# Kernel optimization log

Measured on AMD Instinct MI355X. Metric: run time of the kernel, lower is better.

## Reference

```python
import jax, jax.numpy as jnp
import numpy as np

NUM_HEADS = 32
EPS = 1e-5
NEG_INF = -1e9


def _ln(x, g, b):
    m = x.mean(-1, keepdims=True)
    v = ((x - m) ** 2).mean(-1, keepdims=True)
    return (x - m) / jnp.sqrt(v + EPS) * g + b


def setup_inputs() -> dict:
    key = jax.random.key(0)
    ks = jax.random.split(key, 20)
    N, B, D, E, F, L = 512, 2, 768, 256, 3072, 4
    inp = {
        'x': jax.random.normal(ks[0], (N, B, D), jnp.float32),
        'pos': jax.random.normal(ks[1], (B, N, 3), jnp.float32) * 5.0,
        'padding_mask': jnp.broadcast_to(jnp.arange(N)[None, :] >= N - 32, (B, N)),
        'outcell_index': jax.random.randint(ks[2], (B, E), 0, N),
        'expand_pos': jax.random.normal(ks[3], (B, E, 3), jnp.float32) * 5.0,
        'expand_mask': jnp.broadcast_to(jnp.arange(E)[None, :] >= E - 16, (B, E)),
        'vec_project_w': jax.random.normal(ks[4], (D, 3 * D), jnp.float32) * 0.02,
        'ln_x_g': jnp.ones((L, D), jnp.float32),
        'ln_x_b': jnp.zeros((L, D), jnp.float32),
        'ln_vec_g': jnp.ones((L, D), jnp.float32),
        'ln_vec_b': jnp.zeros((L, D), jnp.float32),
        'adaln_x_w': jax.random.normal(ks[5], (L, D, D), jnp.float32) * 0.02,
        'adaln_vecmlp_w': jax.random.normal(ks[6], (L, D, 2 * D), jnp.float32) * 0.02,
        'out_proj_w': jax.random.normal(ks[7], (L, D, D), jnp.float32) * 0.02,
        'vecmlp_norm_g': jnp.ones((L, D), jnp.float32),
        'vecmlp_norm_b': jnp.zeros((L, D), jnp.float32),
        'mlp_w1': jax.random.normal(ks[8], (L, D, F), jnp.float32) * 0.02,
        'mlp_w2': jax.random.normal(ks[9], (L, F, D), jnp.float32) * 0.02,
    }
    return inp


def reference(x, pos, padding_mask, outcell_index, expand_pos, expand_mask,
              vec_project_w, ln_x_g, ln_x_b, ln_vec_g, ln_vec_b,
              adaln_x_w, adaln_vecmlp_w, out_proj_w,
              vecmlp_norm_g, vecmlp_norm_b, mlp_w1, mlp_w2):
    x = jnp.swapaxes(x, 0, 1)  # [B,N,D]
    B, N, D = x.shape
    H = NUM_HEADS
    hd = D // H
    L = ln_x_g.shape[0]

    # --- PBC-expanded pairwise distance bias ---
    epf = jnp.concatenate([pos, expand_pos], axis=1)  # [B,S,3]
    S = epf.shape[1]
    delta = pos[:, :, None, :] - epf[:, None, :, :]   # [B,N,S,3]
    sq = (delta * delta).sum(-1)
    dist = jnp.where(sq > 0, jnp.sqrt(jnp.where(sq > 0, sq, 1.0)), 0.0)
    kpm_full = jnp.concatenate([padding_mask, expand_mask], axis=-1)  # [B,S]
    dist = jnp.where(padding_mask[:, :, None], 1e6, dist)
    dist = jnp.where(kpm_full[:, None, :], 1e6, dist)
    dist = 1.0 / (dist + 1.0)
    # additive attn mask (bias + key-padding -inf), broadcast over heads
    attn_mask = jnp.where(kpm_full[:, None, None, :], NEG_INF, dist[:, None, :, :])  # [B,1,N,S]

    vec = (jax.nn.silu(x) @ vec_project_w).reshape(B, N, 3, D)
    barange = jnp.arange(B)[:, None]
    scale = 1.0 / jnp.sqrt(jnp.float32(3 * hd))

    for l in range(L):
        rx, rv = x, vec
        xl = _ln(x, ln_x_g[l], ln_x_b[l])
        vl = _ln(vec, ln_vec_g[l], ln_vec_b[l])
        scale_x = jax.nn.silu(xl) @ adaln_x_w[l]        # [B,N,D]
        vmod = vl * scale_x[:, :, None, :]              # [B,N,3,D]
        # PBC gather-expanded K/V
        kv_exp = vmod[barange, outcell_index]           # [B,E,3,D]
        kv = jnp.concatenate([vmod, kv_exp], axis=1)    # [B,S,3,D]
        q = vmod.reshape(B, N, 3, H, hd).transpose(0, 3, 1, 2, 4).reshape(B, H, N, 3 * hd)
        k = kv.reshape(B, S, 3, H, hd).transpose(0, 3, 1, 2, 4).reshape(B, H, S, 3 * hd)
        v = k  # q=k=v in this block (same modulated vec)
        k = kv.reshape(B, S, 3, H, hd).transpose(0, 3, 1, 2, 4).reshape(B, H, S, 3 * hd)
        logits = jnp.einsum('bhnd,bhsd->bhns', q, k) * scale + attn_mask
        p = jax.nn.softmax(logits, axis=-1)
        o = jnp.einsum('bhns,bhsd->bhnd', p, v)          # [B,H,N,3hd]
        o = o.transpose(0, 2, 1, 3).reshape(B, N, H, 3, hd).transpose(0, 1, 3, 2, 4).reshape(B, N, 3, D)
        o = o @ out_proj_w[l]
        x = xl + rx
        vec = o + rv
        rx, rv = x, vec
        vm = _ln(vec, vecmlp_norm_g[l], vecmlp_norm_b[l])
        vm = jax.nn.silu(vm @ mlp_w1[l]) @ mlp_w2[l]     # [B,N,3,D]
        ss = jax.nn.silu(vm) @ adaln_vecmlp_w[l]         # [B,N,3,2D]
        sc, sh = jnp.split(ss, 2, axis=-1)
        x = x * sc.sum(-2) + sh.sum(-2) + rx
        vec = vm + rv
    return x, vec
```

## Files before the change

kernel.cpp:

```cpp
#include <hip/hip_runtime.h>

typedef __bf16 bf16_t;
typedef __bf16 bf8   __attribute__((ext_vector_type(8)));
typedef __bf16 bf4   __attribute__((ext_vector_type(4)));
typedef float  f32x4 __attribute__((ext_vector_type(4)));

__device__ __forceinline__ f32x4 mfma16(bf8 a, bf8 b, f32x4 c){
  return __builtin_amdgcn_mfma_f32_16x16x32_bf16(a, b, c, 0, 0, 0);
}
__device__ __forceinline__ float siluf_(float x){ return x / (1.f + __expf(-x)); }

__device__ __forceinline__ void async16(bf16_t* lds, const bf16_t* g){
  __builtin_amdgcn_global_load_lds(
      (const __attribute__((address_space(1))) unsigned int*)g,
      (__attribute__((address_space(3))) unsigned int*)lds, 16, 0, 0);
}

#define SCALE_QK 0.1178511302f

#define WT_VP   0ull
#define WT_AX   3538944ull
#define WT_AV   8257536ull
#define WT_OP   17694720ull
#define WT_M1   22413312ull
#define WT_M2   41287680ull
#define MASKB   60162048ull
#define SILUX   63307776ull
#define SILUXL  64880640ull
#define VLB     66453504ull
#define SCALEX  75890688ull
#define QKHB    79036416ull
#define KVTB    88473600ull
#define OBFB    97910784ull
#define VMLNB   102629376ull
#define H1B     107347968ull
#define SVM2B   126222336ull
#define SSB     130940928ull

struct TD { const float* s; bf16_t* d; int R, C, start, perz; };
struct TPack { TD t[6]; };

__global__ void transpose_all(TPack P)
{
  __shared__ bf16_t tile[64][66];
  const int bid = blockIdx.x;
  int k = 0;
  #pragma unroll
  for (int i = 1; i < 6; ++i) k = (bid >= P.t[i].start) ? i : k;
  const TD td = P.t[k];
  const int loc = bid - td.start;
  const int z = loc / td.perz, tl = loc - z*td.perz;
  const int nct = td.C >> 6;
  const int cx = tl % nct, ry = tl / nct;
  const size_t base = (size_t)z * td.R * td.C;
  const int r0 = ry*64, c0 = cx*64;
  const int tx = threadIdx.x, ty = threadIdx.y;
  #pragma unroll
  for (int j = 0; j < 16; ++j){
    int rr = ty + 4*j;
    tile[rr][tx] = (bf16_t)td.s[base + (size_t)(r0 + rr)*td.C + c0 + tx];
  }
  __syncthreads();
  #pragma unroll
  for (int j = 0; j < 16; ++j){
    int cc = ty + 4*j;
    td.d[base + (size_t)(c0 + cc)*td.R + r0 + tx] = tile[tx][cc];
  }
}

__global__ void mask_kernel(const float* __restrict__ pos, const float* __restrict__ epos,
                            bf16_t* __restrict__ wm)
{
  int i = blockIdx.x * 256 + threadIdx.x;
  int s = i % 768, t = i / 768;
  int n = t % 512, b = t / 512;
  bool kpm = (s < 512) ? (s >= 480) : (s >= 752);
  float o;
  if (kpm) o = 0.f;
  else {
    float d;
    if (n >= 480) d = 1e6f;
    else {
      const float* p = pos + (size_t)(b*512 + n)*3;
      const float* e = (s < 512) ? pos + (size_t)(b*512 + s)*3
                                 : epos + (size_t)(b*256 + (s-512))*3;
      float dx = p[0]-e[0], dy = p[1]-e[1], dz = p[2]-e[2];
      float sq = dx*dx + dy*dy + dz*dz;
      d = sq > 0.f ? sqrtf(sq) : 0.f;
    }
    o = __expf(1.f / (d + 1.f));
  }
  wm[i] = (bf16_t)o;
}

__global__ void xin_kernel(const float* __restrict__ xin, float* __restrict__ x,
                           bf16_t* __restrict__ sx)
{
  int i = blockIdx.x * 256 + threadIdx.x;
  int d = i % 768, t = i / 768;
  int n = t % 512, b = t / 512;
  float v = xin[((size_t)n*2 + b)*768 + d];
  x[i] = v;
  sx[i] = (bf16_t)siluf_(v);
}

__global__ __launch_bounds__(256,2) void ln_kernel(
    const float* __restrict__ in, const float* __restrict__ g, const float* __restrict__ bb,
    float* __restrict__ f32out, int addres, bf16_t* __restrict__ bfout, int dosilu)
{
  const int w = threadIdx.x >> 6, l = threadIdx.x & 63;
  const size_t r = (size_t)blockIdx.x * 4 + w;
  const float* p = in + r * 768;
  float v[12]; float s = 0.f;
  #pragma unroll
  for (int e = 0; e < 12; ++e){ v[e] = p[e*64 + l]; s += v[e]; }
  #pragma unroll
  for (int m = 1; m < 64; m <<= 1) s += __shfl_xor(s, m);
  float mean = s * (1.f/768.f);
  float q = 0.f;
  #pragma unroll
  for (int e = 0; e < 12; ++e){ float d = v[e] - mean; q += d*d; }
  #pragma unroll
  for (int m = 1; m < 64; m <<= 1) q += __shfl_xor(q, m);
  float rstd = rsqrtf(q * (1.f/768.f) + 1e-5f);
  #pragma unroll
  for (int e = 0; e < 12; ++e){
    int col = e*64 + l;
    float o = (v[e] - mean) * rstd * g[col] + bb[col];
    if (f32out) f32out[r*768 + col] = addres ? (o + v[e]) : o;
    if (bfout)  bfout[r*768 + col]  = (bf16_t)(dosilu ? siluf_(o) : o);
  }
}

__global__ __launch_bounds__(256,2) void pack2_kernel(
    const bf16_t* __restrict__ vl, const bf16_t* __restrict__ scx,
    const int* __restrict__ idx, bf16_t* __restrict__ qkh, bf16_t* __restrict__ kvt)
{
  __shared__ bf16_t tile[32*100];
  const int sb = blockIdx.x, bh = blockIdx.y;
  const int b = bh >> 5, h = bh & 31;
  const int tid = threadIdx.x;
  #pragma unroll
  for (int i = 0; i < 12; ++i){
    int e = i*256 + tid;
    int s_l = e / 96, col = e % 96;
    int s = sb*32 + s_l;
    float v = 0.f;
    if (col < 72){
      int n = (s < 512) ? s : idx[b*256 + (s - 512)];
      int c = col / 24, jj = col - c*24;
      int d = h*24 + jj;
      v = (float)vl[((size_t)(b*512 + n)*3 + c)*768 + d]
        * (float)scx[(size_t)(b*512 + n)*768 + d];
    }
    bf16_t bv = (bf16_t)v;
    qkh[((size_t)bh*768 + s)*96 + col] = bv;
    tile[s_l*100 + col] = bv;
  }
  __syncthreads();
  #pragma unroll
  for (int i = 0; i < 12; ++i){
    int f = i*256 + tid;
    int col = f >> 5, s_l = f & 31;
    kvt[((size_t)bh*96 + col)*768 + sb*32 + s_l] = tile[s_l*100 + col];
  }
}

__global__ __launch_bounds__(256,2) void attn_kernel(
    const bf16_t* __restrict__ qkh, const bf16_t* __restrict__ kvt,
    const bf16_t* __restrict__ wm, bf16_t* __restrict__ obf)
{
  __shared__ bf16_t Ks[64*128];
  __shared__ bf16_t Vs[96*72];
  __shared__ bf16_t Ps[64*72];
  const int g = blockIdx.x;
  const int qt = g >> 6, bh = g & 63;
  const int b = bh >> 5, h = bh & 31;
  const int tid = threadIdx.x, w = tid >> 6, l = tid & 63;
  const int lg = l >> 4, lr = l & 15;
  const int qn0 = qt*64 + w*16 + lg*4;

  bf8 aq[3];
  {
    const bf16_t* qb = qkh + ((size_t)bh*768 + qt*64 + w*16 + lr)*96;
    #pragma unroll
    for (int ks = 0; ks < 3; ++ks) aq[ks] = *(const bf8*)(qb + ks*32 + lg*8);
  }

  int klds[3], vlds[3]; size_t kg[3], vg[3];
  #pragma unroll
  for (int it = 0; it < 3; ++it){
    int f = it*256 + tid;
    int r_ = f / 12, c_ = f % 12;
    klds[it] = r_*256 + ((c_*16) ^ ((r_ & 7) << 4));
    kg[it] = ((size_t)bh*768 + r_)*96 + c_*8;
    int vd = f >> 3, vc = (f & 7)*8;
    vlds[it] = vd*72 + vc;
    vg[it] = ((size_t)bh*96 + vd)*768 + vc;
  }

  f32x4 zf = {0.f,0.f,0.f,0.f};
  f32x4 accO[6];
  #pragma unroll
  for (int i = 0; i < 6; ++i) accO[i] = zf;
  float m_r[4], s_r[4];
  #pragma unroll
  for (int r = 0; r < 4; ++r){ m_r[r] = -1e30f; s_r[r] = 0.f; }

  bf8 kr[3], vr[3];
  #pragma unroll
  for (int it = 0; it < 3; ++it){
    kr[it] = *(const bf8*)(qkh + kg[it]);
    vr[it] = *(const bf8*)(kvt + vg[it]);
  }
  #pragma unroll
  for (int it = 0; it < 3; ++it){
    *(bf8*)((char*)Ks + klds[it]) = kr[it];
    *(bf8*)&Vs[vlds[it]] = vr[it];
  }
  __syncthreads();

  const bf16_t* wrow = wm + (size_t)b*512*768;

  for (int t = 0; t < 12; ++t){
    const int s0 = t*64;
    if (t < 11){
      #pragma unroll
      for (int it = 0; it < 3; ++it){
        kr[it] = *(const bf8*)(qkh + kg[it] + (size_t)(s0 + 64)*96);
        vr[it] = *(const bf8*)(kvt + vg[it] + (s0 + 64));
      }
    }
    f32x4 sacc[4];
    __builtin_amdgcn_s_setprio(1);
    #pragma unroll
    for (int sf = 0; sf < 4; ++sf){
      sacc[sf] = zf;
      const int row = sf*16 + lr;
      #pragma unroll
      for (int ks = 0; ks < 3; ++ks){
        bf8 bg = *(const bf8*)((const char*)Ks + row*256 + ((ks*64 + lg*16) ^ ((row & 7) << 4)));
        sacc[sf] = mfma16(aq[ks], bg, sacc[sf]);
      }
    }
    __builtin_amdgcn_s_setprio(0);
    float tm[4];
    #pragma unroll
    for (int r = 0; r < 4; ++r)
      tm[r] = fmaxf(fmaxf(sacc[0][r], sacc[1][r]), fmaxf(sacc[2][r], sacc[3][r]));
    #pragma unroll
    for (int m = 1; m < 16; m <<= 1)
      #pragma unroll
      for (int r = 0; r < 4; ++r) tm[r] = fmaxf(tm[r], __shfl_xor(tm[r], m));
    float al[4], ps[4];
    #pragma unroll
    for (int r = 0; r < 4; ++r){
      float mn = fmaxf(m_r[r], tm[r]);
      al[r] = __expf((m_r[r] - mn)*SCALE_QK);
      m_r[r] = mn; ps[r] = 0.f;
    }
    #pragma unroll
    for (int sf = 0; sf < 4; ++sf)
      #pragma unroll
      for (int r = 0; r < 4; ++r){
        float p = __expf((sacc[sf][r] - m_r[r])*SCALE_QK)
                  * (float)wrow[(size_t)(qn0 + r)*768 + s0 + sf*16 + lr];
        ps[r] += p;
        Ps[(w*16 + lg*4 + r)*72 + sf*16 + lr] = (bf16_t)p;
      }
    #pragma unroll
    for (int m = 1; m < 16; m <<= 1)
      #pragma unroll
      for (int r = 0; r < 4; ++r) ps[r] += __shfl_xor(ps[r], m);
    #pragma unroll
    for (int r = 0; r < 4; ++r) s_r[r] = s_r[r]*al[r] + ps[r];
    #pragma unroll
    for (int df = 0; df < 6; ++df){
      f32x4 tt = accO[df];
      #pragma unroll
      for (int r = 0; r < 4; ++r) tt[r] *= al[r];
      accO[df] = tt;
    }
    __builtin_amdgcn_s_setprio(1);
    #pragma unroll
    for (int k2 = 0; k2 < 2; ++k2){
      bf8 pa = *(const bf8*)&Ps[(w*16 + lr)*72 + k2*32 + lg*8];
      #pragma unroll
      for (int df = 0; df < 6; ++df)
        accO[df] = mfma16(pa, *(const bf8*)&Vs[(df*16 + lr)*72 + k2*32 + lg*8], accO[df]);
    }
    __builtin_amdgcn_s_setprio(0);
    if (t < 11){
      __syncthreads();
      #pragma unroll
      for (int it = 0; it < 3; ++it){
        *(bf8*)((char*)Ks + klds[it]) = kr[it];
        *(bf8*)&Vs[vlds[it]] = vr[it];
      }
      __syncthreads();
    }
  }
  #pragma unroll
  for (int df = 0; df < 6; ++df){
    int dp = df*16 + lr;
    if (dp < 72){
      int c = dp / 24, jj = dp - c*24;
      #pragma unroll
      for (int r = 0; r < 4; ++r){
        float v = accO[df][r] / s_r[r];
        int qn = qn0 + r;
        obf[((size_t)(b*512 + qn)*3 + c)*768 + h*24 + jj] = (bf16_t)v;
      }
    }
  }
}

template<int EPI>
__global__ __launch_bounds__(512,4) void gemm2(
    const bf16_t* __restrict__ A, const bf16_t* __restrict__ Bt,
    float* __restrict__ Cf, bf16_t* __restrict__ Cb,
    int M, int Nn, int K, int Ksub, int ntiles)
{
  __shared__ bf16_t As[128*64];
  __shared__ bf16_t Bs[128*64];
  const int tid = threadIdx.x;
  const int w = tid >> 6, l = tid & 63;
  const int lg = l >> 4, lr = l & 15;
  const int gb = blockIdx.x;
  const int sidx = gb >> 3, xcd = gb & 7;
  const int nt = sidx % ntiles;
  const int mt = xcd + (sidx / ntiles) * 8;
  const int wm = (w >> 2) * 64, wn = (w & 3) * 32;

  const int srow = w*8 + (l >> 3);
  const int scol = (((l & 7) ^ (l >> 3)) << 3);
  const bf16_t* Ab = A  + (size_t)(mt*128) * K;
  const bf16_t* Bb = Bt + (size_t)(nt*128) * K;
  const int kbeg = blockIdx.z * Ksub;

  f32x4 zf = {0.f,0.f,0.f,0.f};
  f32x4 acc[4][2];
  #pragma unroll
  for (int i = 0; i < 4; ++i)
    #pragma unroll
    for (int j = 0; j < 2; ++j) acc[i][j] = zf;

  int offA[4], offB[2];
  #pragma unroll
  for (int i = 0; i < 4; ++i){
    int row = wm + i*16 + lr;
    offA[i] = row*128 + ((lg*16) ^ ((row & 7) << 4));
  }
  #pragma unroll
  for (int j = 0; j < 2; ++j){
    int row = wn + j*16 + lr;
    offB[j] = row*128 + ((lg*16) ^ ((row & 7) << 4));
  }

  for (int k0 = kbeg; k0 < kbeg + Ksub; k0 += 64){
    __syncthreads();
    #pragma unroll
    for (int c = 0; c < 2; ++c){
      async16(&As[c*4096 + w*512], Ab + (size_t)(c*64 + srow)*K + k0 + scol);
      async16(&Bs[c*4096 + w*512], Bb + (size_t)(c*64 + srow)*K + k0 + scol);
    }
    __syncthreads();
    #pragma unroll
    for (int kk = 0; kk < 2; ++kk){
      bf8 af[4], bg[2];
      #pragma unroll
      for (int i = 0; i < 4; ++i)
        af[i] = *(const bf8*)((const char*)As + (offA[i] ^ (kk*64)));
      #pragma unroll
      for (int j = 0; j < 2; ++j)
        bg[j] = *(const bf8*)((const char*)Bs + (offB[j] ^ (kk*64)));
      #pragma unroll
      for (int i = 0; i < 4; ++i)
        #pragma unroll
        for (int j = 0; j < 2; ++j)
          acc[i][j] = mfma16(af[i], bg[j], acc[i][j]);
    }
  }

  const size_t zoff = (EPI == 4) ? (size_t)blockIdx.z * M * Nn : 0;
  #pragma unroll
  for (int i = 0; i < 4; ++i){
    int r0 = mt*128 + wm + i*16 + lg*4;
    #pragma unroll
    for (int j = 0; j < 2; ++j){
      int cc = nt*128 + wn + j*16 + lr;
      #pragma unroll
      for (int r = 0; r < 4; ++r){
        size_t off = (size_t)(r0 + r)*Nn + cc;
        float v = acc[i][j][r];
        if constexpr (EPI == 0)      Cf[off] = v;
        else if constexpr (EPI == 2) Cb[off] = (bf16_t)siluf_(v);
        else if constexpr (EPI == 4) Cf[zoff + off] = v;
        else                         Cb[off] = (bf16_t)v;
      }
    }
  }
}

__global__ void reduce4_bf(const float* __restrict__ p, bf16_t* __restrict__ out)
{
  int i = blockIdx.x * 256 + threadIdx.x;
  const f32x4* p4 = (const f32x4*)p;
  f32x4 a = p4[i], b = p4[i + 196608], c = p4[i + 393216], d = p4[i + 589824];
  bf4 o;
  #pragma unroll
  for (int r = 0; r < 4; ++r) o[r] = (bf16_t)(a[r] + b[r] + c[r] + d[r]);
  ((bf4*)out)[i] = o;
}

__global__ __launch_bounds__(256,2) void redop_ln(
    const float* __restrict__ p, float* __restrict__ vec,
    const float* __restrict__ g, const float* __restrict__ bb,
    bf16_t* __restrict__ vmln)
{
  const int w = threadIdx.x >> 6, l = threadIdx.x & 63;
  const size_t r = (size_t)blockIdx.x * 4 + w;
  float v[12]; float s = 0.f;
  #pragma unroll
  for (int e = 0; e < 12; ++e){
    size_t off = r*768 + e*64 + l;
    float t = vec[off] + p[off] + p[off + 2359296];
    vec[off] = t;
    v[e] = t; s += t;
  }
  #pragma unroll
  for (int m = 1; m < 64; m <<= 1) s += __shfl_xor(s, m);
  float mean = s * (1.f/768.f);
  float q = 0.f;
  #pragma unroll
  for (int e = 0; e < 12; ++e){ float d = v[e] - mean; q += d*d; }
  #pragma unroll
  for (int m = 1; m < 64; m <<= 1) q += __shfl_xor(q, m);
  float rstd = rsqrtf(q * (1.f/768.f) + 1e-5f);
  #pragma unroll
  for (int e = 0; e < 12; ++e){
    int col = e*64 + l;
    vmln[r*768 + col] = (bf16_t)((v[e] - mean) * rstd * g[col] + bb[col]);
  }
}

__global__ void reduce_mlp2(const float* __restrict__ p, float* __restrict__ vec,
                            bf16_t* __restrict__ svm2)
{
  int i = blockIdx.x * 256 + threadIdx.x;
  const f32x4* p4 = (const f32x4*)p;
  f32x4 a = p4[i], b = p4[i + 589824];
  f32x4* v4 = (f32x4*)vec;
  f32x4 vv = v4[i];
  bf4 o;
  #pragma unroll
  for (int r = 0; r < 4; ++r){
    float s = a[r] + b[r];
    vv[r] += s;
    o[r] = (bf16_t)siluf_(s);
  }
  v4[i] = vv;
  ((bf4*)svm2)[i] = o;
}

__global__ __launch_bounds__(256,2) void comb_ln(
    const bf16_t* __restrict__ ss, float* __restrict__ x,
    const float* __restrict__ g, const float* __restrict__ bb,
    bf16_t* __restrict__ siluxl)
{
  const int w = threadIdx.x >> 6, l = threadIdx.x & 63;
  const size_t r = (size_t)blockIdx.x * 4 + w;
  const size_t base = r * 4608;
  float v[12]; float s = 0.f;
  #pragma unroll
  for (int e = 0; e < 12; ++e){
    int col = e*64 + l;
    float sc = (float)ss[base + col] + (float)ss[base + 1536 + col] + (float)ss[base + 3072 + col];
    float sh = (float)ss[base + 768 + col] + (float)ss[base + 2304 + col] + (float)ss[base + 3840 + col];
    float xv = x[r*768 + col]*(1.f + sc) + sh;
    v[e] = xv; s += xv;
  }
  #pragma unroll
  for (int m = 1; m < 64; m <<= 1) s += __shfl_xor(s, m);
  float mean = s * (1.f/768.f);
  float q = 0.f;
  #pragma unroll
  for (int e = 0; e < 12; ++e){ float d = v[e] - mean; q += d*d; }
  #pragma unroll
  for (int m = 1; m < 64; m <<= 1) q += __shfl_xor(q, m);
  float rstd = rsqrtf(q * (1.f/768.f) + 1e-5f);
  #pragma unroll
  for (int e = 0; e < 12; ++e){
    int col = e*64 + l;
    float xl = (v[e] - mean) * rstd * g[col] + bb[col];
    x[r*768 + col] = xl + v[e];
    siluxl[r*768 + col] = (bf16_t)siluf_(xl);
  }
}

__global__ void combine_kernel(const bf16_t* __restrict__ ss, float* __restrict__ x)
{
  int i = blockIdx.x * 256 + threadIdx.x;
  size_t base = (size_t)(i / 768)*4608 + (i % 768);
  float sc = (float)ss[base] + (float)ss[base + 1536] + (float)ss[base + 3072];
  float sh = (float)ss[base + 768] + (float)ss[base + 2304] + (float)ss[base + 3840];
  x[i] = x[i]*(1.f + sc) + sh;
}

extern "C" void kernel_launch(void* const* d_in, const int* in_sizes, int n_in,
                              void* d_out, int out_size, void* d_ws, size_t ws_size,
                              hipStream_t stream)
{
  const float* x_in = (const float*)d_in[0];
  const float* pos  = (const float*)d_in[1];
  const int*   idx  = (const int*)d_in[3];
  const float* epos = (const float*)d_in[4];
  const float* vp_w = (const float*)d_in[6];
  const float* lxg  = (const float*)d_in[7];
  const float* lxb  = (const float*)d_in[8];
  const float* lvg  = (const float*)d_in[9];
  const float* lvb  = (const float*)d_in[10];
  const float* axw  = (const float*)d_in[11];
  const float* avw  = (const float*)d_in[12];
  const float* opw  = (const float*)d_in[13];
  const float* vng  = (const float*)d_in[14];
  const float* vnb  = (const float*)d_in[15];
  const float* w1   = (const float*)d_in[16];
  const float* w2   = (const float*)d_in[17];

  char* ws = (char*)d_ws;
  bf16_t* wt_vp = (bf16_t*)(ws + WT_VP);
  bf16_t* wt_ax = (bf16_t*)(ws + WT_AX);
  bf16_t* wt_av = (bf16_t*)(ws + WT_AV);
  bf16_t* wt_op = (bf16_t*)(ws + WT_OP);
  bf16_t* wt_m1 = (bf16_t*)(ws + WT_M1);
  bf16_t* wt_m2 = (bf16_t*)(ws + WT_M2);
  bf16_t* wmask = (bf16_t*)(ws + MASKB);
  bf16_t* silux = (bf16_t*)(ws + SILUX);
  bf16_t* siluxl= (bf16_t*)(ws + SILUXL);
  bf16_t* vlb   = (bf16_t*)(ws + VLB);
  bf16_t* scxb  = (bf16_t*)(ws + SCALEX);
  bf16_t* qkh   = (bf16_t*)(ws + QKHB);
  bf16_t* kvt   = (bf16_t*)(ws + KVTB);
  float*  part  = (float*)(ws + QKHB);
  bf16_t* obf   = (bf16_t*)(ws + OBFB);
  bf16_t* vmln  = (bf16_t*)(ws + VMLNB);
  bf16_t* h1    = (bf16_t*)(ws + H1B);
  bf16_t* svm2  = (bf16_t*)(ws + SVM2B);
  bf16_t* ssb   = (bf16_t*)(ws + SSB);

  float* x   = (float*)d_out;
  float* vec = x + 786432;

  TPack P;
  P.t[0] = { vp_w, wt_vp, 768, 2304,    0,  432 };
  P.t[1] = { axw,  wt_ax, 768,  768,  432,  144 };
  P.t[2] = { avw,  wt_av, 768, 1536, 1008,  288 };
  P.t[3] = { opw,  wt_op, 768,  768, 2160,  144 };
  P.t[4] = { w1,   wt_m1, 768, 3072, 2736,  576 };
  P.t[5] = { w2,   wt_m2, 3072, 768, 5040,  576 };
  transpose_all<<<7344, dim3(64, 4), 0, stream>>>(P);

  mask_kernel<<<3072, 256, 0, stream>>>(pos, epos, wmask);
  xin_kernel<<<3072, 256, 0, stream>>>(x_in, x, silux);

  gemm2<0><<<dim3(8*18,1,1), 512, 0, stream>>>(silux, wt_vp, vec, nullptr,
                                               1024, 2304, 768, 768, 18);
  ln_kernel<<<256, 256, 0, stream>>>(x, lxg, lxb, x, 1, siluxl, 1);

  for (int l = 0; l < 4; ++l){
    ln_kernel<<<768, 256, 0, stream>>>(vec, lvg + l*768, lvb + l*768, nullptr, 0, vlb, 0);
    gemm2<4><<<dim3(8*6,1,4), 512, 0, stream>>>(siluxl, wt_ax + (size_t)l*768*768, part,
                                                nullptr, 1024, 768, 768, 192, 6);
    reduce4_bf<<<768, 256, 0, stream>>>(part, scxb);
    pack2_kernel<<<dim3(24, 64), 256, 0, stream>>>(vlb, scxb, idx, qkh, kvt);
    attn_kernel<<<512, 256, 0, stream>>>(qkh, kvt, wmask, obf);
    gemm2<4><<<dim3(24*6,1,2), 512, 0, stream>>>(obf, wt_op + (size_t)l*768*768, part,
                                                 nullptr, 3072, 768, 768, 384, 6);
    redop_ln<<<768, 256, 0, stream>>>(part, vec, vng + l*768, vnb + l*768, vmln);
    gemm2<2><<<dim3(24*24,1,1), 512, 0, stream>>>(vmln, wt_m1 + (size_t)l*3072*768, nullptr,
                                                  h1, 3072, 3072, 768, 768, 24);
    gemm2<4><<<dim3(24*6,1,2), 512, 0, stream>>>(h1, wt_m2 + (size_t)l*768*3072, part,
                                                 nullptr, 3072, 768, 3072, 1536, 6);
    reduce_mlp2<<<2304, 256, 0, stream>>>(part, vec, svm2);
    gemm2<5><<<dim3(24*12,1,1), 512, 0, stream>>>(svm2, wt_av + (size_t)l*1536*768, nullptr,
                                                  ssb, 3072, 1536, 768, 768, 12);
    if (l < 3)
      comb_ln<<<256, 256, 0, stream>>>(ssb, x, lxg + (l+1)*768, lxb + (l+1)*768, siluxl);
    else
      combine_kernel<<<3072, 256, 0, stream>>>(ssb, x);
  }
}
```

Measured before the change: 708.4 us.

## Sum silu(vm) over xyz before adaLN GEMM and vectorize weight transpose

Since the scale/shift GEMM is linear and its outputs are summed over the 3 vector components, the silu activations are now summed across components before the GEMM. This cuts that GEMM's M dimension from 3072 to 1024 rows, and the combine kernels read one sc/sh pair instead of three. The weight transpose kernel also switches to float4 loads and 8-wide bf16 stores with a flat 256-thread block. The reordering of the sum and the bf16 rounding slightly changes numerics.

```diff
diff --git a/kernel.cpp b/kernel.cpp
--- a/kernel.cpp
+++ b/kernel.cpp
@@ -54,17 +54,24 @@
   const int cx = tl % nct, ry = tl / nct;
   const size_t base = (size_t)z * td.R * td.C;
   const int r0 = ry*64, c0 = cx*64;
-  const int tx = threadIdx.x, ty = threadIdx.y;
-  #pragma unroll
-  for (int j = 0; j < 16; ++j){
-    int rr = ty + 4*j;
-    tile[rr][tx] = (bf16_t)td.s[base + (size_t)(r0 + rr)*td.C + c0 + tx];
+  const int t = threadIdx.x;
+  #pragma unroll
+  for (int j = 0; j < 4; ++j){
+    int r = (t >> 4) + j*16;
+    int cc = (t & 15) * 4;
+    f32x4 v = *(const f32x4*)(td.s + base + (size_t)(r0 + r)*td.C + c0 + cc);
+    #pragma unroll
+    for (int e = 0; e < 4; ++e) tile[r][cc + e] = (bf16_t)v[e];
   }
   __syncthreads();
   #pragma unroll
-  for (int j = 0; j < 16; ++j){
-    int cc = ty + 4*j;
-    td.d[base + (size_t)(c0 + cc)*td.R + r0 + tx] = tile[tx][cc];
+  for (int j = 0; j < 2; ++j){
+    int sid = j*256 + t;
+    int c = sid >> 3, q = sid & 7;
+    bf8 o;
+    #pragma unroll
+    for (int e = 0; e < 8; ++e) o[e] = tile[q*8 + e][c];
+    *(bf8*)(td.d + base + (size_t)(c0 + c)*td.R + r0 + q*8) = o;
   }
 }
 
@@ -445,22 +452,30 @@
 }
 
 __global__ void reduce_mlp2(const float* __restrict__ p, float* __restrict__ vec,
-                            bf16_t* __restrict__ svm2)
+                            bf16_t* __restrict__ svm2s)
 {
   int i = blockIdx.x * 256 + threadIdx.x;
+  int bn = i / 192, d4 = i % 192;
   const f32x4* p4 = (const f32x4*)p;
-  f32x4 a = p4[i], b = p4[i + 589824];
   f32x4* v4 = (f32x4*)vec;
-  f32x4 vv = v4[i];
+  float acc[4] = {0.f, 0.f, 0.f, 0.f};
+  #pragma unroll
+  for (int c = 0; c < 3; ++c){
+    size_t idx4 = ((size_t)bn*3 + c)*192 + d4;
+    f32x4 a = p4[idx4], b = p4[idx4 + 589824];
+    f32x4 vv = v4[idx4];
+    #pragma unroll
+    for (int r = 0; r < 4; ++r){
+      float s = a[r] + b[r];
+      vv[r] += s;
+      acc[r] += siluf_(s);
+    }
+    v4[idx4] = vv;
+  }
   bf4 o;
   #pragma unroll
-  for (int r = 0; r < 4; ++r){
-    float s = a[r] + b[r];
-    vv[r] += s;
-    o[r] = (bf16_t)siluf_(s);
-  }
-  v4[i] = vv;
-  ((bf4*)svm2)[i] = o;
+  for (int r = 0; r < 4; ++r) o[r] = (bf16_t)acc[r];
+  ((bf4*)svm2s)[i] = o;
 }
 
 __global__ __launch_bounds__(256,2) void comb_ln(
@@ -470,13 +485,13 @@
 {
   const int w = threadIdx.x >> 6, l = threadIdx.x & 63;
   const size_t r = (size_t)blockIdx.x * 4 + w;
-  const size_t base = r * 4608;
+  const size_t base = r * 1536;
   float v[12]; float s = 0.f;
   #pragma unroll
   for (int e = 0; e < 12; ++e){
     int col = e*64 + l;
-    float sc = (float)ss[base + col] + (float)ss[base + 1536 + col] + (float)ss[base + 3072 + col];
-    float sh = (float)ss[base + 768 + col] + (float)ss[base + 2304 + col] + (float)ss[base + 3840 + col];
+    float sc = (float)ss[base + col];
+    float sh = (float)ss[base + 768 + col];
     float xv = x[r*768 + col]*(1.f + sc) + sh;
     v[e] = xv; s += xv;
   }
@@ -501,9 +516,9 @@
 __global__ void combine_kernel(const bf16_t* __restrict__ ss, float* __restrict__ x)
 {
   int i = blockIdx.x * 256 + threadIdx.x;
-  size_t base = (size_t)(i / 768)*4608 + (i % 768);
-  float sc = (float)ss[base] + (float)ss[base + 1536] + (float)ss[base + 3072];
-  float sh = (float)ss[base + 768] + (float)ss[base + 2304] + (float)ss[base + 3840];
+  size_t base = (size_t)(i / 768)*1536 + (i % 768);
+  float sc = (float)ss[base];
+  float sh = (float)ss[base + 768];
   x[i] = x[i]*(1.f + sc) + sh;
 }
 
@@ -546,7 +561,7 @@
   bf16_t* obf   = (bf16_t*)(ws + OBFB);
   bf16_t* vmln  = (bf16_t*)(ws + VMLNB);
   bf16_t* h1    = (bf16_t*)(ws + H1B);
-  bf16_t* svm2  = (bf16_t*)(ws + SVM2B);
+  bf16_t* svm2s = (bf16_t*)(ws + SVM2B);
   bf16_t* ssb   = (bf16_t*)(ws + SSB);
 
   float* x   = (float*)d_out;
@@ -559,7 +574,7 @@
   P.t[3] = { opw,  wt_op, 768,  768, 2160,  144 };
   P.t[4] = { w1,   wt_m1, 768, 3072, 2736,  576 };
   P.t[5] = { w2,   wt_m2, 3072, 768, 5040,  576 };
-  transpose_all<<<7344, dim3(64, 4), 0, stream>>>(P);
+  transpose_all<<<7344, 256, 0, stream>>>(P);
 
   mask_kernel<<<3072, 256, 0, stream>>>(pos, epos, wmask);
   xin_kernel<<<3072, 256, 0, stream>>>(x_in, x, silux);
@@ -582,9 +597,9 @@
                                                   h1, 3072, 3072, 768, 768, 24);
     gemm2<4><<<dim3(24*6,1,2), 512, 0, stream>>>(h1, wt_m2 + (size_t)l*768*3072, part,
                                                  nullptr, 3072, 768, 3072, 1536, 6);
-    reduce_mlp2<<<2304, 256, 0, stream>>>(part, vec, svm2);
-    gemm2<5><<<dim3(24*12,1,1), 512, 0, stream>>>(svm2, wt_av + (size_t)l*1536*768, nullptr,
-                                                  ssb, 3072, 1536, 768, 768, 12);
+    reduce_mlp2<<<768, 256, 0, stream>>>(part, vec, svm2s);
+    gemm2<5><<<dim3(8*12,1,1), 512, 0, stream>>>(svm2s, wt_av + (size_t)l*1536*768, nullptr,
+                                                 ssb, 1024, 1536, 768, 768, 12);
     if (l < 3)
       comb_ln<<<256, 256, 0, stream>>>(ssb, x, lxg + (l+1)*768, lxb + (l+1)*768, siluxl);
     else
```

After: 696.8 us. No clear change (-1.6%).
